# Kernel optimization log

Hardware: AMD Instinct MI355X
Metric: run time of the kernel (lower is better)

## Reference

```python
import jax, jax.numpy as jnp
import numpy as np


def _sample_plane(plane, coords):
    """torch.nn.functional.grid_sample, mode='bilinear', padding_mode='zeros',
    align_corners=True.  plane: [C,H,W]; coords: [N,2] with (x,y) in [-1,1]
    (x indexes W, y indexes H, as in torch grid convention).  Returns [N,C]."""
    C, H, W = plane.shape
    x = (coords[:, 0] + 1.0) * 0.5 * (W - 1)
    y = (coords[:, 1] + 1.0) * 0.5 * (H - 1)
    x0f = jnp.floor(x); y0f = jnp.floor(y)
    wx = x - x0f; wy = y - y0f

    def corner(yi, xi):
        valid = (xi >= 0) & (xi < W) & (yi >= 0) & (yi < H)
        xc = jnp.clip(xi, 0, W - 1).astype(jnp.int32)
        yc = jnp.clip(yi, 0, H - 1).astype(jnp.int32)
        return plane[:, yc, xc] * valid.astype(plane.dtype)  # [C,N]

    v00 = corner(y0f, x0f)
    v01 = corner(y0f, x0f + 1)
    v10 = corner(y0f + 1, x0f)
    v11 = corner(y0f + 1, x0f + 1)
    out = (v00 * (1 - wx) * (1 - wy) + v01 * wx * (1 - wy)
           + v10 * (1 - wx) * wy + v11 * wx * wy)
    return out.T  # [N,C]


_sample_batched = jax.vmap(_sample_plane)  # [B,C,H,W],[B,N,2] -> [B,N,C]


def setup_inputs() -> dict:
    key = jax.random.key(0)
    ks = jax.random.split(key, 8)
    B, N, C, R = 4, 131072, 32, 256
    triplanes = jax.random.normal(ks[0], (B, 3, C, R, R), jnp.float32) * 0.1
    coordinates = jax.random.uniform(ks[1], (B, N, 3), jnp.float32, -1.0, 1.0)
    # MLP weights ~ frequency_init(30) / first_layer_sine_init scales
    w0 = jax.random.uniform(ks[2], (128, C), jnp.float32, -1.0 / C, 1.0 / C)
    b0 = jnp.zeros((128,), jnp.float32)
    s1 = np.sqrt(6.0 / 128) / 30.0
    w1 = jax.random.uniform(ks[3], (128, 128), jnp.float32, -s1, s1)
    b1 = jnp.zeros((128,), jnp.float32)
    w2 = jax.random.uniform(ks[4], (1, 128), jnp.float32, -s1, s1)
    b2 = jnp.zeros((1,), jnp.float32)
    return {"triplanes": triplanes, "coordinates": coordinates,
            "w0": w0, "b0": b0, "w1": w1, "b1": b1, "w2": w2, "b2": b2}


def reference(triplanes, coordinates, w0, b0, w1, b1, w2, b2):
    # triplanes: [B,3,C,R,R]; coordinates: [B,N,3]
    xy = _sample_batched(triplanes[:, 0], coordinates[..., 0:2])   # (x,y)
    yz = _sample_batched(triplanes[:, 1], coordinates[..., 1:3])   # (y,z)
    xz = _sample_batched(triplanes[:, 2], coordinates[..., 0::2])  # (x,z)
    features = xy * yz * xz  # aggregate_fn == 'prod'; [B,N,C]
    h = jax.nn.relu(jnp.einsum('bnc,hc->bnh', features, w0) + b0)
    h = jax.nn.relu(jnp.einsum('bnh,gh->bng', h, w1) + b1)
    return jnp.einsum('bng,og->bno', h, w2) + b2  # [B,N,1]
```

## Files before the change

kernel.cpp:

```cpp
#include <hip/hip_runtime.h>
#include <hip/hip_bf16.h>
#include <cstddef>

#define RES 256
#define NCH 32
#define NPT 131072
#define NB  4

typedef _Float16 half8 __attribute__((ext_vector_type(8)));
typedef _Float16 half4 __attribute__((ext_vector_type(4)));
typedef float    f32x4 __attribute__((ext_vector_type(4)));

#define FEAT_STRIDE 40
#define H0_STRIDE   136

#define STAGE_SLOT  1024
#define STAGE_BYTES (24 * STAGE_SLOT)

typedef __attribute__((address_space(3))) void        lds_void_t;
typedef __attribute__((address_space(1))) const void  gbl_cvoid_t;

__global__ __launch_bounds__(256) void transpose_prep_kernel(
    const float* __restrict__ in,
    const float* __restrict__ w0, const float* __restrict__ w1,
    _Float16* __restrict__ out,
    _Float16* __restrict__ w0h, _Float16* __restrict__ w1h)
{
    const int bp = blockIdx.y;
    const int t  = threadIdx.x;

    if (bp == 12) {
        const int i = blockIdx.x * 256 + t;
        if (i < 128 * NCH)  w0h[i] = (_Float16)(w0[i] * 16.0f);
        if (i < 128 * 128)  w1h[i] = (_Float16)w1[i];
        return;
    }

    __shared__ _Float16 tileh[NCH][RES + 8];
    const int y = blockIdx.x;

    const float4* src4 = (const float4*)(in + (size_t)bp * NCH * RES * RES);
    const int lane64 = t & 63;
    const int cq     = t >> 6;
    #pragma unroll
    for (int i = 0; i < 8; ++i) {
        const int c = cq * 8 + i;
        const float4 v = src4[(size_t)c * (RES * RES / 4) + y * (RES / 4) + lane64];
        half4 h = { (_Float16)v.x, (_Float16)v.y, (_Float16)v.z, (_Float16)v.w };
        *(half4*)&tileh[c][lane64 * 4] = h;
    }
    __syncthreads();

    _Float16* dst = out + ((size_t)bp * RES * RES + (size_t)y * RES) * NCH;
    const int x = t;
    #pragma unroll
    for (int cg = 0; cg < 4; ++cg) {
        half8 h;
        #pragma unroll
        for (int k = 0; k < 8; ++k)
            h[k] = tileh[cg * 8 + k][x];
        *(half8*)&dst[(size_t)x * NCH + cg * 8] = h;
    }
}

__global__ __launch_bounds__(64, 1) void fused_kernel(
    const _Float16* __restrict__ planesT,
    const float* __restrict__ coords,
    const _Float16* __restrict__ w0h,
    const _Float16* __restrict__ w1h,
    const float* __restrict__ b0, const float* __restrict__ b1,
    const float* __restrict__ w2, const float* __restrict__ b2,
    float* __restrict__ out)
{
    __shared__ __align__(16) unsigned char stage[STAGE_BYTES];
    _Float16* wbase = (_Float16*)stage;

    const int tid  = threadIdx.x;
    const int l15  = tid & 15;
    const int quad = tid >> 4;

    {
        const int p  = tid >> 1;
        const int hf = tid & 1;
        const int gp = blockIdx.x * 32 + p;
        const int b  = gp >> 17;
        const float cx = coords[(size_t)gp * 3 + 0];
        const float cy = coords[(size_t)gp * 3 + 1];
        const float cz = coords[(size_t)gp * 3 + 2];

        int   offs[12];
        float wgt[12];
        #pragma unroll
        for (int pl = 0; pl < 3; ++pl) {
            const float u = (pl == 0) ? cx : (pl == 1) ? cy : cx;
            const float v = (pl == 0) ? cy : cz;

            const float fx = (u + 1.0f) * 0.5f * (RES - 1);
            const float fy = (v + 1.0f) * 0.5f * (RES - 1);
            const float x0f = floorf(fx), y0f = floorf(fy);
            const float wx = fx - x0f, wy = fy - y0f;
            const int x0 = (int)x0f, y0 = (int)y0f;
            const bool vx1 = (x0 + 1) < RES;
            const bool vy1 = (y0 + 1) < RES;
            const int x1 = vx1 ? x0 + 1 : RES - 1;
            const int y1 = vy1 ? y0 + 1 : RES - 1;

            float w00 = (1.0f - wx) * (1.0f - wy);
            float w01 = wx * (1.0f - wy);
            float w10 = (1.0f - wx) * wy;
            float w11 = wx * wy;
            if (!vx1) { w01 = 0.0f; w11 = 0.0f; }
            if (!vy1) { w10 = 0.0f; w11 = 0.0f; }

            const int pbase = ((b * 3 + pl) << 21) + (hf << 4);
            offs[pl * 4 + 0] = pbase + (y0 << 13) + (x0 << 5);
            offs[pl * 4 + 1] = pbase + (y0 << 13) + (x1 << 5);
            offs[pl * 4 + 2] = pbase + (y1 << 13) + (x0 << 5);
            offs[pl * 4 + 3] = pbase + (y1 << 13) + (x1 << 5);
            wgt[pl * 4 + 0] = w00; wgt[pl * 4 + 1] = w01;
            wgt[pl * 4 + 2] = w10; wgt[pl * 4 + 3] = w11;
        }

        #pragma unroll
        for (int i = 0; i < 12; ++i) {
            const _Float16* cp = planesT + (size_t)(unsigned)offs[i];
            __builtin_amdgcn_global_load_lds(
                (gbl_cvoid_t*)cp,
                (lds_void_t*)(stage + (2 * i) * STAGE_SLOT), 16, 0, 0);
            __builtin_amdgcn_global_load_lds(
                (gbl_cvoid_t*)(cp + 8),
                (lds_void_t*)(stage + (2 * i + 1) * STAGE_SLOT), 16, 0, 0);
        }
        asm volatile("s_waitcnt vmcnt(0)" ::: "memory");
        __builtin_amdgcn_sched_barrier(0);

        float prod[16];
        #pragma unroll
        for (int pl = 0; pl < 3; ++pl) {
            half8 c0[4], c1[4];
            #pragma unroll
            for (int c = 0; c < 4; ++c) {
                c0[c] = *(const half8*)&stage[(pl * 8 + 2 * c)     * STAGE_SLOT + tid * 16];
                c1[c] = *(const half8*)&stage[(pl * 8 + 2 * c + 1) * STAGE_SLOT + tid * 16];
            }
            #pragma unroll
            for (int k = 0; k < 8; ++k) {
                const float t0 =
                    fmaf((float)c0[3][k], wgt[pl*4+3],
                    fmaf((float)c0[2][k], wgt[pl*4+2],
                    fmaf((float)c0[1][k], wgt[pl*4+1],
                         (float)c0[0][k] * wgt[pl*4+0])));
                const float t1 =
                    fmaf((float)c1[3][k], wgt[pl*4+3],
                    fmaf((float)c1[2][k], wgt[pl*4+2],
                    fmaf((float)c1[1][k], wgt[pl*4+1],
                         (float)c1[0][k] * wgt[pl*4+0])));
                if (pl == 0) { prod[k] = t0;  prod[8 + k] = t1; }
                else         { prod[k] *= t0; prod[8 + k] *= t1; }
            }
        }

        half8 o0, o1;
        #pragma unroll
        for (int k = 0; k < 8; ++k) {
            o0[k] = (_Float16)(prod[k]     * 256.0f);
            o1[k] = (_Float16)(prod[8 + k] * 256.0f);
        }
        *(half8*)&wbase[p * FEAT_STRIDE + hf * 16 + 0] = o0;
        *(half8*)&wbase[p * FEAT_STRIDE + hf * 16 + 8] = o1;
    }

    half8 a0[2];
    #pragma unroll
    for (int mt = 0; mt < 2; ++mt)
        a0[mt] = *(const half8*)&wbase[(mt * 16 + l15) * FEAT_STRIDE + quad * 8];

    float b0v[8], b1v[8], w2s[8];
    #pragma unroll
    for (int nt = 0; nt < 8; ++nt) {
        b0v[nt] = b0[nt * 16 + l15] * 4096.0f;
        b1v[nt] = b1[nt * 16 + l15] * 4096.0f;
        w2s[nt] = w2[nt * 16 + l15] * (1.0f / 4096.0f);
    }

    #pragma unroll 1
    for (int nt = 0; nt < 8; ++nt) {
        const half8 bfr = *(const half8*)&w0h[(nt * 16 + l15) * NCH + quad * 8];
        f32x4 acc[2];
        #pragma unroll
        for (int mt = 0; mt < 2; ++mt) {
            acc[mt] = (f32x4){0.f, 0.f, 0.f, 0.f};
            acc[mt] = __builtin_amdgcn_mfma_f32_16x16x32_f16(
                a0[mt], bfr, acc[mt], 0, 0, 0);
        }
        #pragma unroll
        for (int mt = 0; mt < 2; ++mt)
            #pragma unroll
            for (int r = 0; r < 4; ++r) {
                const float hval = fmaxf(acc[mt][r] + b0v[nt], 0.0f);
                wbase[(mt * 16 + quad * 4 + r) * H0_STRIDE + nt * 16 + l15]
                    = (_Float16)hval;
            }
    }

    half8 a1[2][4];
    #pragma unroll
    for (int mt = 0; mt < 2; ++mt)
        #pragma unroll
        for (int ks = 0; ks < 4; ++ks)
            a1[mt][ks] = *(const half8*)
                &wbase[(mt * 16 + l15) * H0_STRIDE + ks * 32 + quad * 8];

    float part[2][4];
    #pragma unroll
    for (int mt = 0; mt < 2; ++mt)
        #pragma unroll
        for (int r = 0; r < 4; ++r) part[mt][r] = 0.0f;

    #pragma unroll 2
    for (int nt = 0; nt < 8; ++nt) {
        f32x4 acc[2];
        #pragma unroll
        for (int mt = 0; mt < 2; ++mt) acc[mt] = (f32x4){0.f, 0.f, 0.f, 0.f};
        #pragma unroll
        for (int ks = 0; ks < 4; ++ks) {
            const half8 bfr = *(const half8*)
                &w1h[(nt * 16 + l15) * 128 + ks * 32 + quad * 8];
            #pragma unroll
            for (int mt = 0; mt < 2; ++mt)
                acc[mt] = __builtin_amdgcn_mfma_f32_16x16x32_f16(
                    a1[mt][ks], bfr, acc[mt], 0, 0, 0);
        }
        #pragma unroll
        for (int mt = 0; mt < 2; ++mt)
            #pragma unroll
            for (int r = 0; r < 4; ++r)
                part[mt][r] = fmaf(w2s[nt], fmaxf(acc[mt][r] + b1v[nt], 0.0f),
                                   part[mt][r]);
    }

    #pragma unroll
    for (int mt = 0; mt < 2; ++mt)
        #pragma unroll
        for (int r = 0; r < 4; ++r) {
            float s = part[mt][r];
            s += __shfl_xor(s, 1);
            s += __shfl_xor(s, 2);
            s += __shfl_xor(s, 4);
            s += __shfl_xor(s, 8);
            part[mt][r] = s;
        }

    if (l15 == 0) {
        const float bias2 = b2[0];
        const int base = blockIdx.x * 32;
        #pragma unroll
        for (int mt = 0; mt < 2; ++mt)
            #pragma unroll
            for (int r = 0; r < 4; ++r)
                out[base + mt * 16 + quad * 4 + r] = part[mt][r] + bias2;
    }
}

__global__ __launch_bounds__(256) void fused_fallback(
    const float* __restrict__ planes, const float* __restrict__ coords,
    const float* __restrict__ w0, const float* __restrict__ b0,
    const float* __restrict__ w1, const float* __restrict__ b1,
    const float* __restrict__ w2, const float* __restrict__ b2,
    float* __restrict__ out)
{
    const int t = blockIdx.x * 256 + threadIdx.x;
    const int b = t >> 17;
    const float cx = coords[(size_t)t * 3 + 0];
    const float cy = coords[(size_t)t * 3 + 1];
    const float cz = coords[(size_t)t * 3 + 2];
    float feat[NCH];
    #pragma unroll
    for (int p = 0; p < 3; ++p) {
        const float u = (p == 0) ? cx : (p == 1) ? cy : cx;
        const float v = (p == 0) ? cy : cz;
        const float fx = (u + 1.0f) * 0.5f * (RES - 1);
        const float fy = (v + 1.0f) * 0.5f * (RES - 1);
        const float x0f = floorf(fx), y0f = floorf(fy);
        const float wx = fx - x0f, wy = fy - y0f;
        const int x0 = (int)x0f, y0 = (int)y0f;
        const bool vx1 = (x0 + 1) < RES, vy1 = (y0 + 1) < RES;
        const int x1 = vx1 ? x0 + 1 : RES - 1;
        const int y1 = vy1 ? y0 + 1 : RES - 1;
        float w00 = (1.0f - wx) * (1.0f - wy), w01 = wx * (1.0f - wy);
        float w10 = (1.0f - wx) * wy, w11 = wx * wy;
        if (!vx1) { w01 = 0.0f; w11 = 0.0f; }
        if (!vy1) { w10 = 0.0f; w11 = 0.0f; }
        const float* base = planes + (size_t)(b * 3 + p) * NCH * RES * RES;
        const float* p00 = base + (size_t)y0 * RES + x0;
        const float* p01 = base + (size_t)y0 * RES + x1;
        const float* p10 = base + (size_t)y1 * RES + x0;
        const float* p11 = base + (size_t)y1 * RES + x1;
        #pragma unroll
        for (int c = 0; c < NCH; ++c) {
            const size_t off = (size_t)c * RES * RES;
            float s = p00[off] * w00;
            s = fmaf(p01[off], w01, s);
            s = fmaf(p10[off], w10, s);
            s = fmaf(p11[off], w11, s);
            if (p == 0) feat[c] = s; else feat[c] *= s;
        }
    }
    float h0[128];
    #pragma unroll
    for (int g = 0; g < 128; ++g) {
        const float* wr = w0 + g * NCH;
        float aA = b0[g], aB = 0.0f;
        #pragma unroll
        for (int c = 0; c < NCH; c += 2) {
            aA = fmaf(wr[c], feat[c], aA);
            aB = fmaf(wr[c + 1], feat[c + 1], aB);
        }
        h0[g] = fmaxf(aA + aB, 0.0f);
    }
    float o = b2[0];
    for (int g = 0; g < 128; ++g) {
        const float* wr = w1 + g * 128;
        float aA = b1[g], aB = 0.0f, aC = 0.0f, aD = 0.0f;
        #pragma unroll
        for (int h = 0; h < 128; h += 4) {
            aA = fmaf(wr[h], h0[h], aA);
            aB = fmaf(wr[h + 1], h0[h + 1], aB);
            aC = fmaf(wr[h + 2], h0[h + 2], aC);
            aD = fmaf(wr[h + 3], h0[h + 3], aD);
        }
        o = fmaf(fmaxf((aA + aB) + (aC + aD), 0.0f), w2[g], o);
    }
    out[t] = o;
}

extern "C" void kernel_launch(void* const* d_in, const int* in_sizes, int n_in,
                              void* d_out, int out_size, void* d_ws, size_t ws_size,
                              hipStream_t stream)
{
    const float* trip   = (const float*)d_in[0];
    const float* coords = (const float*)d_in[1];
    const float* w0     = (const float*)d_in[2];
    const float* b0     = (const float*)d_in[3];
    const float* w1     = (const float*)d_in[4];
    const float* b1     = (const float*)d_in[5];
    const float* w2     = (const float*)d_in[6];
    const float* b2     = (const float*)d_in[7];
    float* out = (float*)d_out;

    const size_t planesTBytes = (size_t)NB * 3 * RES * RES * NCH * 2;
    const size_t w0hBytes = 128 * NCH * 2;
    const size_t w1hBytes = 128 * 128 * 2;
    const size_t needed = planesTBytes + w0hBytes + w1hBytes;

    if (ws_size >= needed) {
        _Float16* planesT = (_Float16*)d_ws;
        _Float16* w0h     = (_Float16*)((char*)d_ws + planesTBytes);
        _Float16* w1h     = (_Float16*)((char*)d_ws + planesTBytes + w0hBytes);

        transpose_prep_kernel<<<dim3(RES, NB * 3 + 1), 256, 0, stream>>>(
            trip, w0, w1, planesT, w0h, w1h);
        fused_kernel<<<(NB * NPT) / 32, 64, 0, stream>>>(
            planesT, coords, w0h, w1h, b0, b1, w2, b2, out);
    } else {
        fused_fallback<<<(NB * NPT) / 256, 256, 0, stream>>>(
            trip, coords, w0, b0, w1, b1, w2, b2, out);
    }
}
```

Baseline: 290.9 us.

## Software-pipeline gathers across chunks with double-buffered LDS staging per block

Each block now processes eight 32-point chunks in sequence instead of one. The next chunk's global-to-LDS corner gathers are issued before the current chunk's interpolation and MLP run, using two LDS buffers and a partial vmcnt wait. W0 fragments and biases are loaded into registers once per block instead of once per chunk. This aims to hide gather latency and amortise per-block setup, but it doubles LDS per block and cuts the grid eight-fold, which reduces the number of waves available to the hardware to hide latency itself.

```diff
diff --git a/kernel.cpp b/kernel.cpp
--- a/kernel.cpp
+++ b/kernel.cpp
@@ -6,6 +6,8 @@
 #define NCH 32
 #define NPT 131072
 #define NB  4
+
+#define CHUNKS 8
 
 typedef _Float16 half8 __attribute__((ext_vector_type(8)));
 typedef _Float16 half4 __attribute__((ext_vector_type(4)));
@@ -60,6 +62,190 @@
         for (int k = 0; k < 8; ++k)
             h[k] = tileh[cg * 8 + k][x];
         *(half8*)&dst[(size_t)x * NCH + cg * 8] = h;
+    }
+}
+
+__device__ __forceinline__ void load_coords3(
+    const float* __restrict__ coords, int gp, float* c3)
+{
+    c3[0] = coords[(size_t)gp * 3 + 0];
+    c3[1] = coords[(size_t)gp * 3 + 1];
+    c3[2] = coords[(size_t)gp * 3 + 2];
+}
+
+__device__ __forceinline__ void calc_corners(
+    float cx, float cy, float cz, int b, int hf, int* offs, float* wgt)
+{
+    #pragma unroll
+    for (int pl = 0; pl < 3; ++pl) {
+        const float u = (pl == 0) ? cx : (pl == 1) ? cy : cx;
+        const float v = (pl == 0) ? cy : cz;
+
+        const float fx = (u + 1.0f) * 0.5f * (RES - 1);
+        const float fy = (v + 1.0f) * 0.5f * (RES - 1);
+        const float x0f = floorf(fx), y0f = floorf(fy);
+        const float wx = fx - x0f, wy = fy - y0f;
+        const int x0 = (int)x0f, y0 = (int)y0f;
+        const bool vx1 = (x0 + 1) < RES;
+        const bool vy1 = (y0 + 1) < RES;
+        const int x1 = vx1 ? x0 + 1 : RES - 1;
+        const int y1 = vy1 ? y0 + 1 : RES - 1;
+
+        float w00 = (1.0f - wx) * (1.0f - wy);
+        float w01 = wx * (1.0f - wy);
+        float w10 = (1.0f - wx) * wy;
+        float w11 = wx * wy;
+        if (!vx1) { w01 = 0.0f; w11 = 0.0f; }
+        if (!vy1) { w10 = 0.0f; w11 = 0.0f; }
+
+        const int pbase = ((b * 3 + pl) << 21) + (hf << 4);
+        offs[pl * 4 + 0] = pbase + (y0 << 13) + (x0 << 5);
+        offs[pl * 4 + 1] = pbase + (y0 << 13) + (x1 << 5);
+        offs[pl * 4 + 2] = pbase + (y1 << 13) + (x0 << 5);
+        offs[pl * 4 + 3] = pbase + (y1 << 13) + (x1 << 5);
+        wgt[pl * 4 + 0] = w00; wgt[pl * 4 + 1] = w01;
+        wgt[pl * 4 + 2] = w10; wgt[pl * 4 + 3] = w11;
+    }
+}
+
+__device__ __forceinline__ void issue_gathers(
+    const _Float16* __restrict__ planesT, const int* offs, unsigned char* stg)
+{
+    #pragma unroll
+    for (int i = 0; i < 12; ++i) {
+        const _Float16* cp = planesT + (size_t)(unsigned)offs[i];
+        __builtin_amdgcn_global_load_lds(
+            (gbl_cvoid_t*)cp,
+            (lds_void_t*)(stg + (2 * i) * STAGE_SLOT), 16, 0, 0);
+        __builtin_amdgcn_global_load_lds(
+            (gbl_cvoid_t*)(cp + 8),
+            (lds_void_t*)(stg + (2 * i + 1) * STAGE_SLOT), 16, 0, 0);
+    }
+}
+
+__device__ __forceinline__ void compute_chunk(
+    unsigned char* stg, const float* wgt,
+    const half8* w0r, const float* b0v, const float* b1v, const float* w2s,
+    const _Float16* __restrict__ w1h, float bias2, int outbase,
+    int tid, int l15, int quad, int p, int hf,
+    float* __restrict__ out)
+{
+    _Float16* wbase = (_Float16*)stg;
+
+    float prod[16];
+    #pragma unroll
+    for (int pl = 0; pl < 3; ++pl) {
+        half8 c0[4], c1[4];
+        #pragma unroll
+        for (int c = 0; c < 4; ++c) {
+            c0[c] = *(const half8*)&stg[(pl * 8 + 2 * c)     * STAGE_SLOT + tid * 16];
+            c1[c] = *(const half8*)&stg[(pl * 8 + 2 * c + 1) * STAGE_SLOT + tid * 16];
+        }
+        #pragma unroll
+        for (int k = 0; k < 8; ++k) {
+            const float t0 =
+                fmaf((float)c0[3][k], wgt[pl*4+3],
+                fmaf((float)c0[2][k], wgt[pl*4+2],
+                fmaf((float)c0[1][k], wgt[pl*4+1],
+                     (float)c0[0][k] * wgt[pl*4+0])));
+            const float t1 =
+                fmaf((float)c1[3][k], wgt[pl*4+3],
+                fmaf((float)c1[2][k], wgt[pl*4+2],
+                fmaf((float)c1[1][k], wgt[pl*4+1],
+                     (float)c1[0][k] * wgt[pl*4+0])));
+            if (pl == 0) { prod[k] = t0;  prod[8 + k] = t1; }
+            else         { prod[k] *= t0; prod[8 + k] *= t1; }
+        }
+    }
+
+    half8 o0, o1;
+    #pragma unroll
+    for (int k = 0; k < 8; ++k) {
+        o0[k] = (_Float16)(prod[k]     * 256.0f);
+        o1[k] = (_Float16)(prod[8 + k] * 256.0f);
+    }
+    *(half8*)&wbase[p * FEAT_STRIDE + hf * 16 + 0] = o0;
+    *(half8*)&wbase[p * FEAT_STRIDE + hf * 16 + 8] = o1;
+
+    half8 a0[2];
+    #pragma unroll
+    for (int mt = 0; mt < 2; ++mt)
+        a0[mt] = *(const half8*)&wbase[(mt * 16 + l15) * FEAT_STRIDE + quad * 8];
+
+    #pragma unroll 1
+    for (int nt = 0; nt < 8; ++nt) {
+        const half8 bfr = w0r[nt];
+        f32x4 acc[2];
+        #pragma unroll
+        for (int mt = 0; mt < 2; ++mt) {
+            acc[mt] = (f32x4){0.f, 0.f, 0.f, 0.f};
+            acc[mt] = __builtin_amdgcn_mfma_f32_16x16x32_f16(
+                a0[mt], bfr, acc[mt], 0, 0, 0);
+        }
+        #pragma unroll
+        for (int mt = 0; mt < 2; ++mt)
+            #pragma unroll
+            for (int r = 0; r < 4; ++r) {
+                const float hval = fmaxf(acc[mt][r] + b0v[nt], 0.0f);
+                wbase[(mt * 16 + quad * 4 + r) * H0_STRIDE + nt * 16 + l15]
+                    = (_Float16)hval;
+            }
+    }
+
+    half8 a1[2][4];
+    #pragma unroll
+    for (int mt = 0; mt < 2; ++mt)
+        #pragma unroll
+        for (int ks = 0; ks < 4; ++ks)
+            a1[mt][ks] = *(const half8*)
+                &wbase[(mt * 16 + l15) * H0_STRIDE + ks * 32 + quad * 8];
+
+    float part[2][4];
+    #pragma unroll
+    for (int mt = 0; mt < 2; ++mt)
+        #pragma unroll
+        for (int r = 0; r < 4; ++r) part[mt][r] = 0.0f;
+
+    #pragma unroll 2
+    for (int nt = 0; nt < 8; ++nt) {
+        f32x4 acc[2];
+        #pragma unroll
+        for (int mt = 0; mt < 2; ++mt) acc[mt] = (f32x4){0.f, 0.f, 0.f, 0.f};
+        #pragma unroll
+        for (int ks = 0; ks < 4; ++ks) {
+            const half8 bfr = *(const half8*)
+                &w1h[(nt * 16 + l15) * 128 + ks * 32 + quad * 8];
+            #pragma unroll
+            for (int mt = 0; mt < 2; ++mt)
+                acc[mt] = __builtin_amdgcn_mfma_f32_16x16x32_f16(
+                    a1[mt][ks], bfr, acc[mt], 0, 0, 0);
+        }
+        #pragma unroll
+        for (int mt = 0; mt < 2; ++mt)
+            #pragma unroll
+            for (int r = 0; r < 4; ++r)
+                part[mt][r] = fmaf(w2s[nt], fmaxf(acc[mt][r] + b1v[nt], 0.0f),
+                                   part[mt][r]);
+    }
+
+    #pragma unroll
+    for (int mt = 0; mt < 2; ++mt)
+        #pragma unroll
+        for (int r = 0; r < 4; ++r) {
+            float s = part[mt][r];
+            s += __shfl_xor(s, 1);
+            s += __shfl_xor(s, 2);
+            s += __shfl_xor(s, 4);
+            s += __shfl_xor(s, 8);
+            part[mt][r] = s;
+        }
+
+    if (l15 == 0) {
+        #pragma unroll
+        for (int mt = 0; mt < 2; ++mt)
+            #pragma unroll
+            for (int r = 0; r < 4; ++r)
+                out[outbase + mt * 16 + quad * 4 + r] = part[mt][r] + bias2;
     }
 }
 
@@ -72,194 +258,64 @@
     const float* __restrict__ w2, const float* __restrict__ b2,
     float* __restrict__ out)
 {
-    __shared__ __align__(16) unsigned char stage[STAGE_BYTES];
-    _Float16* wbase = (_Float16*)stage;
+    __shared__ __align__(16) unsigned char stageA[STAGE_BYTES];
+    __shared__ __align__(16) unsigned char stageB[STAGE_BYTES];
 
     const int tid  = threadIdx.x;
     const int l15  = tid & 15;
     const int quad = tid >> 4;
-
-    {
-        const int p  = tid >> 1;
-        const int hf = tid & 1;
-        const int gp = blockIdx.x * 32 + p;
-        const int b  = gp >> 17;
-        const float cx = coords[(size_t)gp * 3 + 0];
-        const float cy = coords[(size_t)gp * 3 + 1];
-        const float cz = coords[(size_t)gp * 3 + 2];
-
-        int   offs[12];
-        float wgt[12];
-        #pragma unroll
-        for (int pl = 0; pl < 3; ++pl) {
-            const float u = (pl == 0) ? cx : (pl == 1) ? cy : cx;
-            const float v = (pl == 0) ? cy : cz;
-
-            const float fx = (u + 1.0f) * 0.5f * (RES - 1);
-            const float fy = (v + 1.0f) * 0.5f * (RES - 1);
-            const float x0f = floorf(fx), y0f = floorf(fy);
-            const float wx = fx - x0f, wy = fy - y0f;
-            const int x0 = (int)x0f, y0 = (int)y0f;
-            const bool vx1 = (x0 + 1) < RES;
-            const bool vy1 = (y0 + 1) < RES;
-            const int x1 = vx1 ? x0 + 1 : RES - 1;
-            const int y1 = vy1 ? y0 + 1 : RES - 1;
-
-            float w00 = (1.0f - wx) * (1.0f - wy);
-            float w01 = wx * (1.0f - wy);
-            float w10 = (1.0f - wx) * wy;
-            float w11 = wx * wy;
-            if (!vx1) { w01 = 0.0f; w11 = 0.0f; }
-            if (!vy1) { w10 = 0.0f; w11 = 0.0f; }
-
-            const int pbase = ((b * 3 + pl) << 21) + (hf << 4);
-            offs[pl * 4 + 0] = pbase + (y0 << 13) + (x0 << 5);
-            offs[pl * 4 + 1] = pbase + (y0 << 13) + (x1 << 5);
-            offs[pl * 4 + 2] = pbase + (y1 << 13) + (x0 << 5);
-            offs[pl * 4 + 3] = pbase + (y1 << 13) + (x1 << 5);
-            wgt[pl * 4 + 0] = w00; wgt[pl * 4 + 1] = w01;
-            wgt[pl * 4 + 2] = w10; wgt[pl * 4 + 3] = w11;
-        }
-
-        #pragma unroll
-        for (int i = 0; i < 12; ++i) {
-            const _Float16* cp = planesT + (size_t)(unsigned)offs[i];
-            __builtin_amdgcn_global_load_lds(
-                (gbl_cvoid_t*)cp,
-                (lds_void_t*)(stage + (2 * i) * STAGE_SLOT), 16, 0, 0);
-            __builtin_amdgcn_global_load_lds(
-                (gbl_cvoid_t*)(cp + 8),
-                (lds_void_t*)(stage + (2 * i + 1) * STAGE_SLOT), 16, 0, 0);
-        }
-        asm volatile("s_waitcnt vmcnt(0)" ::: "memory");
-        __builtin_amdgcn_sched_barrier(0);
-
-        float prod[16];
-        #pragma unroll
-        for (int pl = 0; pl < 3; ++pl) {
-            half8 c0[4], c1[4];
-            #pragma unroll
-            for (int c = 0; c < 4; ++c) {
-                c0[c] = *(const half8*)&stage[(pl * 8 + 2 * c)     * STAGE_SLOT + tid * 16];
-                c1[c] = *(const half8*)&stage[(pl * 8 + 2 * c + 1) * STAGE_SLOT + tid * 16];
-            }
-            #pragma unroll
-            for (int k = 0; k < 8; ++k) {
-                const float t0 =
-                    fmaf((float)c0[3][k], wgt[pl*4+3],
-                    fmaf((float)c0[2][k], wgt[pl*4+2],
-                    fmaf((float)c0[1][k], wgt[pl*4+1],
-                         (float)c0[0][k] * wgt[pl*4+0])));
-                const float t1 =
-                    fmaf((float)c1[3][k], wgt[pl*4+3],
-                    fmaf((float)c1[2][k], wgt[pl*4+2],
-                    fmaf((float)c1[1][k], wgt[pl*4+1],
-                         (float)c1[0][k] * wgt[pl*4+0])));
-                if (pl == 0) { prod[k] = t0;  prod[8 + k] = t1; }
-                else         { prod[k] *= t0; prod[8 + k] *= t1; }
-            }
-        }
-
-        half8 o0, o1;
-        #pragma unroll
-        for (int k = 0; k < 8; ++k) {
-            o0[k] = (_Float16)(prod[k]     * 256.0f);
-            o1[k] = (_Float16)(prod[8 + k] * 256.0f);
-        }
-        *(half8*)&wbase[p * FEAT_STRIDE + hf * 16 + 0] = o0;
-        *(half8*)&wbase[p * FEAT_STRIDE + hf * 16 + 8] = o1;
-    }
-
-    half8 a0[2];
-    #pragma unroll
-    for (int mt = 0; mt < 2; ++mt)
-        a0[mt] = *(const half8*)&wbase[(mt * 16 + l15) * FEAT_STRIDE + quad * 8];
-
+    const int p    = tid >> 1;
+    const int hf   = tid & 1;
+    const int chunk0 = blockIdx.x * CHUNKS;
+
+    half8 w0r[8];
     float b0v[8], b1v[8], w2s[8];
     #pragma unroll
     for (int nt = 0; nt < 8; ++nt) {
+        w0r[nt] = *(const half8*)&w0h[(nt * 16 + l15) * NCH + quad * 8];
         b0v[nt] = b0[nt * 16 + l15] * 4096.0f;
         b1v[nt] = b1[nt * 16 + l15] * 4096.0f;
         w2s[nt] = w2[nt * 16 + l15] * (1.0f / 4096.0f);
     }
+    const float bias2 = b2[0];
+
+    float cA[3], cB[3];
+    float wgtA[12], wgtB[12];
+    int   offs[12];
+
+    load_coords3(coords, (chunk0 + 0) * 32 + p, cA);
+    calc_corners(cA[0], cA[1], cA[2], ((chunk0 + 0) * 32 + p) >> 17, hf,
+                 offs, wgtA);
+    load_coords3(coords, (chunk0 + 1) * 32 + p, cB);
+    issue_gathers(planesT, offs, stageA);
+
+#define STEP_FULL(C, CUR, NXT, WCUR, WNXT, CO_NEXT, CO_LOAD)                   \
+    {                                                                          \
+        const int cnx = (C) + 1;                                               \
+        calc_corners(CO_NEXT[0], CO_NEXT[1], CO_NEXT[2],                       \
+                     ((chunk0 + cnx) * 32 + p) >> 17, hf, offs, WNXT);         \
+        const int cpre = ((C) + 2 < CHUNKS) ? (C) + 2 : CHUNKS - 1;            \
+        load_coords3(coords, (chunk0 + cpre) * 32 + p, CO_LOAD);               \
+        issue_gathers(planesT, offs, NXT);                                     \
+        asm volatile("s_waitcnt vmcnt(27)" ::: "memory");                      \
+        __builtin_amdgcn_sched_barrier(0);                                     \
+        compute_chunk(CUR, WCUR, w0r, b0v, b1v, w2s, w1h, bias2,               \
+                      (chunk0 + (C)) * 32, tid, l15, quad, p, hf, out);        \
+    }
 
     #pragma unroll 1
-    for (int nt = 0; nt < 8; ++nt) {
-        const half8 bfr = *(const half8*)&w0h[(nt * 16 + l15) * NCH + quad * 8];
-        f32x4 acc[2];
-        #pragma unroll
-        for (int mt = 0; mt < 2; ++mt) {
-            acc[mt] = (f32x4){0.f, 0.f, 0.f, 0.f};
-            acc[mt] = __builtin_amdgcn_mfma_f32_16x16x32_f16(
-                a0[mt], bfr, acc[mt], 0, 0, 0);
-        }
-        #pragma unroll
-        for (int mt = 0; mt < 2; ++mt)
-            #pragma unroll
-            for (int r = 0; r < 4; ++r) {
-                const float hval = fmaxf(acc[mt][r] + b0v[nt], 0.0f);
-                wbase[(mt * 16 + quad * 4 + r) * H0_STRIDE + nt * 16 + l15]
-                    = (_Float16)hval;
-            }
-    }
-
-    half8 a1[2][4];
-    #pragma unroll
-    for (int mt = 0; mt < 2; ++mt)
-        #pragma unroll
-        for (int ks = 0; ks < 4; ++ks)
-            a1[mt][ks] = *(const half8*)
-                &wbase[(mt * 16 + l15) * H0_STRIDE + ks * 32 + quad * 8];
-
-    float part[2][4];
-    #pragma unroll
-    for (int mt = 0; mt < 2; ++mt)
-        #pragma unroll
-        for (int r = 0; r < 4; ++r) part[mt][r] = 0.0f;
-
-    #pragma unroll 2
-    for (int nt = 0; nt < 8; ++nt) {
-        f32x4 acc[2];
-        #pragma unroll
-        for (int mt = 0; mt < 2; ++mt) acc[mt] = (f32x4){0.f, 0.f, 0.f, 0.f};
-        #pragma unroll
-        for (int ks = 0; ks < 4; ++ks) {
-            const half8 bfr = *(const half8*)
-                &w1h[(nt * 16 + l15) * 128 + ks * 32 + quad * 8];
-            #pragma unroll
-            for (int mt = 0; mt < 2; ++mt)
-                acc[mt] = __builtin_amdgcn_mfma_f32_16x16x32_f16(
-                    a1[mt][ks], bfr, acc[mt], 0, 0, 0);
-        }
-        #pragma unroll
-        for (int mt = 0; mt < 2; ++mt)
-            #pragma unroll
-            for (int r = 0; r < 4; ++r)
-                part[mt][r] = fmaf(w2s[nt], fmaxf(acc[mt][r] + b1v[nt], 0.0f),
-                                   part[mt][r]);
-    }
-
-    #pragma unroll
-    for (int mt = 0; mt < 2; ++mt)
-        #pragma unroll
-        for (int r = 0; r < 4; ++r) {
-            float s = part[mt][r];
-            s += __shfl_xor(s, 1);
-            s += __shfl_xor(s, 2);
-            s += __shfl_xor(s, 4);
-            s += __shfl_xor(s, 8);
-            part[mt][r] = s;
-        }
-
-    if (l15 == 0) {
-        const float bias2 = b2[0];
-        const int base = blockIdx.x * 32;
-        #pragma unroll
-        for (int mt = 0; mt < 2; ++mt)
-            #pragma unroll
-            for (int r = 0; r < 4; ++r)
-                out[base + mt * 16 + quad * 4 + r] = part[mt][r] + bias2;
-    }
+    for (int cc = 0; cc < (CHUNKS - 2) / 2; ++cc) {
+        const int c0 = 2 * cc;
+        STEP_FULL(c0,     stageA, stageB, wgtA, wgtB, cB, cA);
+        STEP_FULL(c0 + 1, stageB, stageA, wgtB, wgtA, cA, cB);
+    }
+    STEP_FULL(CHUNKS - 2, stageA, stageB, wgtA, wgtB, cB, cA);
+#undef STEP_FULL
+
+    asm volatile("s_waitcnt vmcnt(0)" ::: "memory");
+    __builtin_amdgcn_sched_barrier(0);
+    compute_chunk(stageB, wgtB, w0r, b0v, b1v, w2s, w1h, bias2,
+                  (chunk0 + CHUNKS - 1) * 32, tid, l15, quad, p, hf, out);
 }
 
 __global__ __launch_bounds__(256) void fused_fallback(
@@ -360,7 +416,7 @@
 
         transpose_prep_kernel<<<dim3(RES, NB * 3 + 1), 256, 0, stream>>>(
             trip, w0, w1, planesT, w0h, w1h);
-        fused_kernel<<<(NB * NPT) / 32, 64, 0, stream>>>(
+        fused_kernel<<<(NB * NPT) / (32 * CHUNKS), 64, 0, stream>>>(
             planesT, coords, w0h, w1h, b0, b1, w2, b2, out);
     } else {
         fused_fallback<<<(NB * NPT) / 256, 256, 0, stream>>>(
```

Result: slower. 798.2 us (+174.4%).

## Shrink LDS staging to one plane slot and hoist W0 fragment loads

Applied to the files above, without the earlier changes.

The kernel now stages one plane's corner gathers at a time in a reused 8 KB LDS slot instead of holding all three planes at once (24 KB). The next plane's loads are issued right after the current plane is read into registers, so interpolation overlaps the following gather. The smaller LDS footprint should let more single-wave blocks fit per CU, giving more latency hiding. W0 fragments and biases are also loaded up front in registers. The trade-off is three serialized wait rounds per wave instead of one fully batched gather, which lowers memory-level parallelism within each wave, plus extra register pressure.

```diff
diff --git a/kernel.cpp b/kernel.cpp
--- a/kernel.cpp
+++ b/kernel.cpp
@@ -15,7 +15,7 @@
 #define H0_STRIDE   136
 
 #define STAGE_SLOT  1024
-#define STAGE_BYTES (24 * STAGE_SLOT)
+#define LDS_BYTES   8704
 
 typedef __attribute__((address_space(3))) void        lds_void_t;
 typedef __attribute__((address_space(1))) const void  gbl_cvoid_t;
@@ -60,6 +60,86 @@
         for (int k = 0; k < 8; ++k)
             h[k] = tileh[cg * 8 + k][x];
         *(half8*)&dst[(size_t)x * NCH + cg * 8] = h;
+    }
+}
+
+__device__ __forceinline__ void calc_plane(
+    int pl, float cx, float cy, float cz, int b, int hf,
+    int* __restrict__ offs, float* __restrict__ wgt)
+{
+    const float u = (pl == 0) ? cx : (pl == 1) ? cy : cx;
+    const float v = (pl == 0) ? cy : cz;
+
+    const float fx = (u + 1.0f) * 0.5f * (RES - 1);
+    const float fy = (v + 1.0f) * 0.5f * (RES - 1);
+    const float x0f = floorf(fx), y0f = floorf(fy);
+    const float wx = fx - x0f, wy = fy - y0f;
+    const int x0 = (int)x0f, y0 = (int)y0f;
+    const bool vx1 = (x0 + 1) < RES;
+    const bool vy1 = (y0 + 1) < RES;
+    const int x1 = vx1 ? x0 + 1 : RES - 1;
+    const int y1 = vy1 ? y0 + 1 : RES - 1;
+
+    float w00 = (1.0f - wx) * (1.0f - wy);
+    float w01 = wx * (1.0f - wy);
+    float w10 = (1.0f - wx) * wy;
+    float w11 = wx * wy;
+    if (!vx1) { w01 = 0.0f; w11 = 0.0f; }
+    if (!vy1) { w10 = 0.0f; w11 = 0.0f; }
+
+    const int pbase = ((b * 3 + pl) << 21) + (hf << 4);
+    offs[pl * 4 + 0] = pbase + (y0 << 13) + (x0 << 5);
+    offs[pl * 4 + 1] = pbase + (y0 << 13) + (x1 << 5);
+    offs[pl * 4 + 2] = pbase + (y1 << 13) + (x0 << 5);
+    offs[pl * 4 + 3] = pbase + (y1 << 13) + (x1 << 5);
+    wgt[pl * 4 + 0] = w00; wgt[pl * 4 + 1] = w01;
+    wgt[pl * 4 + 2] = w10; wgt[pl * 4 + 3] = w11;
+}
+
+__device__ __forceinline__ void issue_plane(
+    const _Float16* __restrict__ planesT, const int* offs4,
+    unsigned char* stg)
+{
+    #pragma unroll
+    for (int c = 0; c < 4; ++c) {
+        const _Float16* cp = planesT + (size_t)(unsigned)offs4[c];
+        __builtin_amdgcn_global_load_lds(
+            (gbl_cvoid_t*)cp,
+            (lds_void_t*)(stg + (2 * c) * STAGE_SLOT), 16, 0, 0);
+        __builtin_amdgcn_global_load_lds(
+            (gbl_cvoid_t*)(cp + 8),
+            (lds_void_t*)(stg + (2 * c + 1) * STAGE_SLOT), 16, 0, 0);
+    }
+}
+
+__device__ __forceinline__ void read_slots(
+    const unsigned char* stg, int tid, half8* c0, half8* c1)
+{
+    #pragma unroll
+    for (int c = 0; c < 4; ++c) {
+        c0[c] = *(const half8*)&stg[(2 * c)     * STAGE_SLOT + tid * 16];
+        c1[c] = *(const half8*)&stg[(2 * c + 1) * STAGE_SLOT + tid * 16];
+    }
+}
+
+__device__ __forceinline__ void interp_plane(
+    int pl, const half8* c0, const half8* c1, const float* wgt,
+    float* __restrict__ prod)
+{
+    #pragma unroll
+    for (int k = 0; k < 8; ++k) {
+        const float t0 =
+            fmaf((float)c0[3][k], wgt[pl*4+3],
+            fmaf((float)c0[2][k], wgt[pl*4+2],
+            fmaf((float)c0[1][k], wgt[pl*4+1],
+                 (float)c0[0][k] * wgt[pl*4+0])));
+        const float t1 =
+            fmaf((float)c1[3][k], wgt[pl*4+3],
+            fmaf((float)c1[2][k], wgt[pl*4+2],
+            fmaf((float)c1[1][k], wgt[pl*4+1],
+                 (float)c1[0][k] * wgt[pl*4+0])));
+        if (pl == 0) { prod[k] = t0;  prod[8 + k] = t1; }
+        else         { prod[k] *= t0; prod[8 + k] *= t1; }
     }
 }
 
@@ -72,120 +152,81 @@
     const float* __restrict__ w2, const float* __restrict__ b2,
     float* __restrict__ out)
 {
-    __shared__ __align__(16) unsigned char stage[STAGE_BYTES];
+    __shared__ __align__(16) unsigned char stage[LDS_BYTES];
     _Float16* wbase = (_Float16*)stage;
 
     const int tid  = threadIdx.x;
     const int l15  = tid & 15;
     const int quad = tid >> 4;
-
-    {
-        const int p  = tid >> 1;
-        const int hf = tid & 1;
-        const int gp = blockIdx.x * 32 + p;
-        const int b  = gp >> 17;
-        const float cx = coords[(size_t)gp * 3 + 0];
-        const float cy = coords[(size_t)gp * 3 + 1];
-        const float cz = coords[(size_t)gp * 3 + 2];
-
-        int   offs[12];
-        float wgt[12];
-        #pragma unroll
-        for (int pl = 0; pl < 3; ++pl) {
-            const float u = (pl == 0) ? cx : (pl == 1) ? cy : cx;
-            const float v = (pl == 0) ? cy : cz;
-
-            const float fx = (u + 1.0f) * 0.5f * (RES - 1);
-            const float fy = (v + 1.0f) * 0.5f * (RES - 1);
-            const float x0f = floorf(fx), y0f = floorf(fy);
-            const float wx = fx - x0f, wy = fy - y0f;
-            const int x0 = (int)x0f, y0 = (int)y0f;
-            const bool vx1 = (x0 + 1) < RES;
-            const bool vy1 = (y0 + 1) < RES;
-            const int x1 = vx1 ? x0 + 1 : RES - 1;
-            const int y1 = vy1 ? y0 + 1 : RES - 1;
-
-            float w00 = (1.0f - wx) * (1.0f - wy);
-            float w01 = wx * (1.0f - wy);
-            float w10 = (1.0f - wx) * wy;
-            float w11 = wx * wy;
-            if (!vx1) { w01 = 0.0f; w11 = 0.0f; }
-            if (!vy1) { w10 = 0.0f; w11 = 0.0f; }
-
-            const int pbase = ((b * 3 + pl) << 21) + (hf << 4);
-            offs[pl * 4 + 0] = pbase + (y0 << 13) + (x0 << 5);
-            offs[pl * 4 + 1] = pbase + (y0 << 13) + (x1 << 5);
-            offs[pl * 4 + 2] = pbase + (y1 << 13) + (x0 << 5);
-            offs[pl * 4 + 3] = pbase + (y1 << 13) + (x1 << 5);
-            wgt[pl * 4 + 0] = w00; wgt[pl * 4 + 1] = w01;
-            wgt[pl * 4 + 2] = w10; wgt[pl * 4 + 3] = w11;
-        }
-
-        #pragma unroll
-        for (int i = 0; i < 12; ++i) {
-            const _Float16* cp = planesT + (size_t)(unsigned)offs[i];
-            __builtin_amdgcn_global_load_lds(
-                (gbl_cvoid_t*)cp,
-                (lds_void_t*)(stage + (2 * i) * STAGE_SLOT), 16, 0, 0);
-            __builtin_amdgcn_global_load_lds(
-                (gbl_cvoid_t*)(cp + 8),
-                (lds_void_t*)(stage + (2 * i + 1) * STAGE_SLOT), 16, 0, 0);
-        }
-        asm volatile("s_waitcnt vmcnt(0)" ::: "memory");
-        __builtin_amdgcn_sched_barrier(0);
-
-        float prod[16];
-        #pragma unroll
-        for (int pl = 0; pl < 3; ++pl) {
-            half8 c0[4], c1[4];
-            #pragma unroll
-            for (int c = 0; c < 4; ++c) {
-                c0[c] = *(const half8*)&stage[(pl * 8 + 2 * c)     * STAGE_SLOT + tid * 16];
-                c1[c] = *(const half8*)&stage[(pl * 8 + 2 * c + 1) * STAGE_SLOT + tid * 16];
-            }
-            #pragma unroll
-            for (int k = 0; k < 8; ++k) {
-                const float t0 =
-                    fmaf((float)c0[3][k], wgt[pl*4+3],
-                    fmaf((float)c0[2][k], wgt[pl*4+2],
-                    fmaf((float)c0[1][k], wgt[pl*4+1],
-                         (float)c0[0][k] * wgt[pl*4+0])));
-                const float t1 =
-                    fmaf((float)c1[3][k], wgt[pl*4+3],
-                    fmaf((float)c1[2][k], wgt[pl*4+2],
-                    fmaf((float)c1[1][k], wgt[pl*4+1],
-                         (float)c1[0][k] * wgt[pl*4+0])));
-                if (pl == 0) { prod[k] = t0;  prod[8 + k] = t1; }
-                else         { prod[k] *= t0; prod[8 + k] *= t1; }
-            }
-        }
-
-        half8 o0, o1;
-        #pragma unroll
-        for (int k = 0; k < 8; ++k) {
-            o0[k] = (_Float16)(prod[k]     * 256.0f);
-            o1[k] = (_Float16)(prod[8 + k] * 256.0f);
-        }
-        *(half8*)&wbase[p * FEAT_STRIDE + hf * 16 + 0] = o0;
-        *(half8*)&wbase[p * FEAT_STRIDE + hf * 16 + 8] = o1;
-    }
-
-    half8 a0[2];
-    #pragma unroll
-    for (int mt = 0; mt < 2; ++mt)
-        a0[mt] = *(const half8*)&wbase[(mt * 16 + l15) * FEAT_STRIDE + quad * 8];
-
+    const int p    = tid >> 1;
+    const int hf   = tid & 1;
+
+    const int gp = blockIdx.x * 32 + p;
+    const int b  = gp >> 17;
+    const float cx = coords[(size_t)gp * 3 + 0];
+    const float cy = coords[(size_t)gp * 3 + 1];
+    const float cz = coords[(size_t)gp * 3 + 2];
+
+    half8 w0r[8];
     float b0v[8], b1v[8], w2s[8];
     #pragma unroll
     for (int nt = 0; nt < 8; ++nt) {
+        w0r[nt] = *(const half8*)&w0h[(nt * 16 + l15) * NCH + quad * 8];
         b0v[nt] = b0[nt * 16 + l15] * 4096.0f;
         b1v[nt] = b1[nt * 16 + l15] * 4096.0f;
         w2s[nt] = w2[nt * 16 + l15] * (1.0f / 4096.0f);
     }
+    const float bias2 = b2[0];
+    __builtin_amdgcn_sched_barrier(0);
+
+    int   offs[12];
+    float wgt[12];
+    calc_plane(0, cx, cy, cz, b, hf, offs, wgt);
+    issue_plane(planesT, offs + 0, stage);
+    calc_plane(1, cx, cy, cz, b, hf, offs, wgt);
+    calc_plane(2, cx, cy, cz, b, hf, offs, wgt);
+
+    float prod[16];
+    half8 c0[4], c1[4];
+
+    asm volatile("s_waitcnt vmcnt(0)" ::: "memory");
+    __builtin_amdgcn_sched_barrier(0);
+    read_slots(stage, tid, c0, c1);
+    asm volatile("s_waitcnt lgkmcnt(0)" ::: "memory");
+    __builtin_amdgcn_sched_barrier(0);
+    issue_plane(planesT, offs + 4, stage);
+    interp_plane(0, c0, c1, wgt, prod);
+
+    asm volatile("s_waitcnt vmcnt(0)" ::: "memory");
+    __builtin_amdgcn_sched_barrier(0);
+    read_slots(stage, tid, c0, c1);
+    asm volatile("s_waitcnt lgkmcnt(0)" ::: "memory");
+    __builtin_amdgcn_sched_barrier(0);
+    issue_plane(planesT, offs + 8, stage);
+    interp_plane(1, c0, c1, wgt, prod);
+
+    asm volatile("s_waitcnt vmcnt(0)" ::: "memory");
+    __builtin_amdgcn_sched_barrier(0);
+    read_slots(stage, tid, c0, c1);
+    interp_plane(2, c0, c1, wgt, prod);
+
+    half8 o0, o1;
+    #pragma unroll
+    for (int k = 0; k < 8; ++k) {
+        o0[k] = (_Float16)(prod[k]     * 256.0f);
+        o1[k] = (_Float16)(prod[8 + k] * 256.0f);
+    }
+    *(half8*)&wbase[p * FEAT_STRIDE + hf * 16 + 0] = o0;
+    *(half8*)&wbase[p * FEAT_STRIDE + hf * 16 + 8] = o1;
+
+    half8 a0[2];
+    #pragma unroll
+    for (int mt = 0; mt < 2; ++mt)
+        a0[mt] = *(const half8*)&wbase[(mt * 16 + l15) * FEAT_STRIDE + quad * 8];
 
     #pragma unroll 1
     for (int nt = 0; nt < 8; ++nt) {
-        const half8 bfr = *(const half8*)&w0h[(nt * 16 + l15) * NCH + quad * 8];
+        const half8 bfr = w0r[nt];
         f32x4 acc[2];
         #pragma unroll
         for (int mt = 0; mt < 2; ++mt) {
@@ -252,7 +293,6 @@
         }
 
     if (l15 == 0) {
-        const float bias2 = b2[0];
         const int base = blockIdx.x * 32;
         #pragma unroll
         for (int mt = 0; mt < 2; ++mt)
```

Result: slower. 688.3 us (+136.6%).
